# Kernel optimization log

Hardware: AMD Instinct MI355X
Metric: run time of the kernel (lower is better)

Reference implementation:

```python
import jax, jax.numpy as jnp
import numpy as np

NUM_LAYERS = 2
SHAPES = [(100, 100), (50, 50), (25, 25), (13, 13)]  # (H, W) per level
D, NH, NP, NL = 256, 8, 4, 4
DH = D // NH
DFF = 1024
B = 2
S = sum(h * w for h, w in SHAPES)  # 13294


def layer_norm(x, g, b, eps=1e-5):
    m = x.mean(-1, keepdims=True)
    v = jnp.var(x, axis=-1, keepdims=True)
    return (x - m) * jax.lax.rsqrt(v + eps) * g + b


def get_reference_points(valid_ratios):
    refs = []
    for lvl, (H_, W_) in enumerate(SHAPES):
        ry, rx = jnp.meshgrid(jnp.linspace(0.5, H_ - 0.5, H_),
                              jnp.linspace(0.5, W_ - 0.5, W_), indexing='ij')
        ry = ry.reshape(-1)[None] / (valid_ratios[:, None, lvl, 1] * H_)
        rx = rx.reshape(-1)[None] / (valid_ratios[:, None, lvl, 0] * W_)
        refs.append(jnp.stack([rx, ry], -1))
    ref = jnp.concatenate(refs, 1)                      # [B, S, 2]
    return ref[:, :, None] * valid_ratios[:, None]      # [B, S, NL, 2]


def sample_level(value_l, H_, W_, loc):
    # value_l: [B, nH, H*W, Dh]; loc: [B, Q, nH, P, 2] normalized in [0,1]
    x = loc[..., 0] * W_ - 0.5
    y = loc[..., 1] * H_ - 0.5
    x0 = jnp.floor(x)
    y0 = jnp.floor(y)
    Bq, Q = loc.shape[0], loc.shape[1]
    acc = 0.
    corners = ((x0, y0, (x0 + 1 - x) * (y0 + 1 - y)),
               (x0 + 1, y0, (x - x0) * (y0 + 1 - y)),
               (x0, y0 + 1, (x0 + 1 - x) * (y - y0)),
               (x0 + 1, y0 + 1, (x - x0) * (y - y0)))
    for xi, yi, w in corners:  # zero-padding grid_sample: invalid corners contribute 0
        valid = (xi >= 0) & (xi <= W_ - 1) & (yi >= 0) & (yi <= H_ - 1)
        idx = (jnp.clip(yi, 0, H_ - 1) * W_ + jnp.clip(xi, 0, W_ - 1)).astype(jnp.int32)
        idx = jnp.transpose(idx, (0, 2, 1, 3)).reshape(Bq, NH, Q * NP)
        g = jnp.take_along_axis(value_l, idx[..., None], axis=2)  # [B,nH,Q*P,Dh]
        wv = jnp.transpose((w * valid).astype(value_l.dtype), (0, 2, 1, 3)).reshape(Bq, NH, Q * NP)
        acc = acc + g * wv[..., None]
    return acc.reshape(Bq, NH, Q, NP, DH)


def msda(query, ref, src, W_val, b_val, W_off, b_off, W_attn, b_attn, W_out, b_out):
    Bq, Q = query.shape[:2]
    value = (src @ W_val + b_val).reshape(Bq, S, NH, DH)
    off = (query @ W_off + b_off).reshape(Bq, Q, NH, NL, NP, 2)
    attn = jax.nn.softmax((query @ W_attn + b_attn).reshape(Bq, Q, NH, NL * NP), -1)
    attn = attn.reshape(Bq, Q, NH, NL, NP)
    normalizer = jnp.array([[w, h] for h, w in SHAPES], dtype=query.dtype)  # [NL,2] (x,y)
    loc = ref[:, :, None, :, None, :] + off / normalizer[None, None, None, :, None, :]
    out = jnp.zeros((Bq, NH, Q, DH), query.dtype)
    start = 0
    for l, (H_, W_) in enumerate(SHAPES):
        v_l = jnp.transpose(value[:, start:start + H_ * W_], (0, 2, 1, 3))  # [B,nH,HW,Dh]
        samp = sample_level(v_l, H_, W_, loc[:, :, :, l])                    # [B,nH,Q,P,Dh]
        w_l = jnp.transpose(attn[:, :, :, l], (0, 2, 1, 3))                  # [B,nH,Q,P]
        out = out + (samp * w_l[..., None]).sum(3)
        start += H_ * W_
    out = jnp.transpose(out, (0, 2, 1, 3)).reshape(Bq, Q, D)
    return out @ W_out + b_out


def setup_inputs() -> dict:
    key = jax.random.key(0)
    ks = jax.random.split(key, 12)
    sc = 0.02
    inp = {
        'src': jax.random.normal(ks[0], (B, S, D), jnp.float32),
        'spatial_shapes': np.array(SHAPES, dtype=np.int64),
        'valid_ratios': jnp.ones((B, NL, 2), jnp.float32),
        'W_off': sc * jax.random.normal(ks[1], (NUM_LAYERS, D, NH * NL * NP * 2), jnp.float32),
        'b_off': jnp.zeros((NUM_LAYERS, NH * NL * NP * 2), jnp.float32),
        'W_attn': sc * jax.random.normal(ks[2], (NUM_LAYERS, D, NH * NL * NP), jnp.float32),
        'b_attn': jnp.zeros((NUM_LAYERS, NH * NL * NP), jnp.float32),
        'W_val': sc * jax.random.normal(ks[3], (NUM_LAYERS, D, D), jnp.float32),
        'b_val': jnp.zeros((NUM_LAYERS, D), jnp.float32),
        'W_out': sc * jax.random.normal(ks[4], (NUM_LAYERS, D, D), jnp.float32),
        'b_out': jnp.zeros((NUM_LAYERS, D), jnp.float32),
        'ln1_g': jnp.ones((NUM_LAYERS, D), jnp.float32),
        'ln1_b': jnp.zeros((NUM_LAYERS, D), jnp.float32),
        'W1': sc * jax.random.normal(ks[5], (NUM_LAYERS, D, DFF), jnp.float32),
        'b1': jnp.zeros((NUM_LAYERS, DFF), jnp.float32),
        'W2': sc * jax.random.normal(ks[6], (NUM_LAYERS, DFF, D), jnp.float32),
        'b2': jnp.zeros((NUM_LAYERS, D), jnp.float32),
        'ln2_g': jnp.ones((NUM_LAYERS, D), jnp.float32),
        'ln2_b': jnp.zeros((NUM_LAYERS, D), jnp.float32),
    }
    return inp


def reference(src, spatial_shapes, valid_ratios, W_off, b_off, W_attn, b_attn,
              W_val, b_val, W_out, b_out, ln1_g, ln1_b, W1, b1, W2, b2, ln2_g, ln2_b):
    # Deformable-DETR encoder stack (dropout=0 / eval mode, pos=None, no padding mask).
    ref = get_reference_points(valid_ratios)  # [B, S, NL, 2]
    x = src
    for i in range(NUM_LAYERS):
        x2 = msda(x, ref, x, W_val[i], b_val[i], W_off[i], b_off[i],
                  W_attn[i], b_attn[i], W_out[i], b_out[i])
        x = layer_norm(x + x2, ln1_g[i], ln1_b[i])
        h = jax.nn.relu(x @ W1[i] + b1[i]) @ W2[i] + b2[i]
        x = layer_norm(x + h, ln2_g[i], ln2_b[i])
    return x
```

## Files before the change

### kernel.cpp

```cpp
#include <hip/hip_runtime.h>
#include <math.h>


#define S_TOT 13294
#define BATCH 2
#define M_TOT (BATCH * S_TOT)
#define M_PAD 26624

typedef __attribute__((ext_vector_type(8))) short short8;
typedef __attribute__((ext_vector_type(4))) float floatx4;
typedef __attribute__((ext_vector_type(2))) float floatx2;

#define AS1C(p) ((const __attribute__((address_space(1))) void*)(p))
#define AS3(p)  ((__attribute__((address_space(3))) void*)(p))

static __device__ __forceinline__ unsigned short f2bf(float x) {
    union { float f; unsigned u; } v; v.f = x;
    unsigned r = v.u + 0x7FFFu + ((v.u >> 16) & 1u);
    return (unsigned short)(r >> 16);
}
static __device__ __forceinline__ float b2f(unsigned short u) {
    union { unsigned u; float f; } v; v.u = (unsigned)u << 16; return v.f;
}
static __device__ __forceinline__ float bflo(unsigned u) {
    union { unsigned u; float f; } v; v.u = u << 16; return v.f;
}
static __device__ __forceinline__ float bfhi(unsigned u) {
    union { unsigned u; float f; } v; v.u = u & 0xFFFF0000u; return v.f;
}
static __device__ __forceinline__ float braw(unsigned u) {
    union { unsigned u; float f; } v; v.u = u; return v.f;
}

template<int TM, bool RELU, bool BF16OUT, bool PROJ>
__global__ __launch_bounds__(256)
void mgemm(const unsigned short* __restrict__ A,
           const unsigned short* __restrict__ BT,
           const float* __restrict__ bias,
           const float* __restrict__ bias2,
           const float* __restrict__ bias3,
           unsigned short* __restrict__ Cb,
           unsigned short* __restrict__ Cb2,
           int M, int N, int K)
{
    constexpr int WM = (TM == 128) ? 2 : 1;
    constexpr int WN = 4 / WM;
    constexpr int MI = TM / (WM * 16);
    constexpr int NI = 128 / (WN * 16);
    __shared__ __align__(16) unsigned short smemA[2 * TM * 32];
    __shared__ __align__(16) unsigned short smemB[2 * 128 * 32];
    const int tid  = threadIdx.x;
    const int lane = tid & 63;
    const int w    = tid >> 6;
    const int wm   = w % WM, wn = w / WM;
    const int lr   = lane & 15, quad = lane >> 4;
    const int bm   = blockIdx.y * TM;
    const int bn   = blockIdx.x * 128;

    floatx4 acc[MI][NI];
    #pragma unroll
    for (int i = 0; i < MI; ++i)
        #pragma unroll
        for (int j = 0; j < NI; ++j)
            acc[i][j] = (floatx4){0.f, 0.f, 0.f, 0.f};

    const int srow = lane >> 2;
    const int selt = (lane & 3) << 3;

    for (int k0 = 0; k0 < K; k0 += 64) {
        #pragma unroll
        for (int c = 0; c < 2; ++c) {
            if (TM == 128) {
                #pragma unroll
                for (int jj = 0; jj < 2; ++jj) {
                    const int j = 2 * w + jj;
                    const unsigned short* ga = A  + (size_t)(bm + j * 16 + srow) * K + k0 + c * 32 + selt;
                    const unsigned short* gb = BT + (size_t)(bn + j * 16 + srow) * K + k0 + c * 32 + selt;
                    __builtin_amdgcn_global_load_lds(AS1C(ga), AS3(smemA + c * (TM * 32) + j * 512), 16, 0, 0);
                    __builtin_amdgcn_global_load_lds(AS1C(gb), AS3(smemB + c * 4096 + j * 512), 16, 0, 0);
                }
            } else {
                const unsigned short* ga = A + (size_t)(bm + w * 16 + srow) * K + k0 + c * 32 + selt;
                __builtin_amdgcn_global_load_lds(AS1C(ga), AS3(smemA + c * (TM * 32) + w * 512), 16, 0, 0);
                #pragma unroll
                for (int jj = 0; jj < 2; ++jj) {
                    const int j = 2 * w + jj;
                    const unsigned short* gb = BT + (size_t)(bn + j * 16 + srow) * K + k0 + c * 32 + selt;
                    __builtin_amdgcn_global_load_lds(AS1C(gb), AS3(smemB + c * 4096 + j * 512), 16, 0, 0);
                }
            }
        }
        __syncthreads();

        #pragma unroll
        for (int c = 0; c < 2; ++c) {
            short8 av[MI], bv[NI];
            #pragma unroll
            for (int mi = 0; mi < MI; ++mi)
                av[mi] = *(const short8*)&smemA[c * (TM * 32) + (wm * MI * 16 + mi * 16 + lr) * 32 + quad * 8];
            #pragma unroll
            for (int ni = 0; ni < NI; ++ni)
                bv[ni] = *(const short8*)&smemB[c * 4096 + (wn * NI * 16 + ni * 16 + lr) * 32 + quad * 8];
            #pragma unroll
            for (int mi = 0; mi < MI; ++mi)
                #pragma unroll
                for (int ni = 0; ni < NI; ++ni)
                    acc[mi][ni] = __builtin_amdgcn_mfma_f32_16x16x32_bf16(
                        av[mi], bv[ni], acc[mi][ni], 0, 0, 0);
        }
        __syncthreads();
    }

    #pragma unroll
    for (int mi = 0; mi < MI; ++mi) {
        #pragma unroll
        for (int ni = 0; ni < NI; ++ni) {
            #pragma unroll
            for (int r = 0; r < 4; ++r) {
                const int row = bm + wm * MI * 16 + mi * 16 + quad * 4 + r;
                const int col = bn + wn * NI * 16 + ni * 16 + lr;
                if (PROJ) {
                    const float bb = (col < 256) ? bias[col]
                                   : (col < 512) ? bias2[col - 256]
                                                 : bias3[col - 512];
                    const float v = acc[mi][ni][r] + bb;
                    if (col < 256) Cb[(size_t)row * 256 + col] = f2bf(v);
                    else           Cb2[(size_t)row * 384 + (col - 256)] = f2bf(v);
                } else {
                    float v = acc[mi][ni][r] + bias[col];
                    if (RELU) v = fmaxf(v, 0.0f);
                    if (BF16OUT) Cb[(size_t)row * N + col] = f2bf(v);
                }
            }
        }
    }
}

template<bool HASF, bool HASB>
__global__ __launch_bounds__(256)
void mgemm_ln(const unsigned short* __restrict__ A,
              const unsigned short* __restrict__ BT,
              const float* __restrict__ bias,
              const unsigned short* __restrict__ R,
              const float* __restrict__ g,
              const float* __restrict__ beta,
              float* __restrict__ outF,
              unsigned short* __restrict__ outB,
              int M, int K)
{
    __shared__ __align__(16) unsigned short smemA[2 * 4096];
    __shared__ __align__(16) unsigned short smemB[2 * 16384];
    const int lane = threadIdx.x & 63;
    const int w    = threadIdx.x >> 6;
    const int lr   = lane & 15, quad = lane >> 4;
    const int bm   = blockIdx.x * 64;
    const int srow = lane >> 2;
    const int selt = (lane & 3) << 3;

    floatx4 acc[4][4];
    #pragma unroll
    for (int i = 0; i < 4; ++i)
        #pragma unroll
        for (int j = 0; j < 4; ++j)
            acc[i][j] = (floatx4){0.f, 0.f, 0.f, 0.f};

    auto stage = [&](int kt, int buf) {
        const int k0 = kt * 64;
        #pragma unroll
        for (int c = 0; c < 2; ++c) {
            const unsigned short* ga = A + (size_t)(bm + w * 16 + srow) * K + k0 + c * 32 + selt;
            __builtin_amdgcn_global_load_lds(AS1C(ga), AS3(smemA + buf * 4096 + c * 2048 + w * 512), 16, 0, 0);
            #pragma unroll
            for (int jj = 0; jj < 4; ++jj) {
                const int j = 4 * w + jj;
                const unsigned short* gb = BT + (size_t)(j * 16 + srow) * K + k0 + c * 32 + selt;
                __builtin_amdgcn_global_load_lds(AS1C(gb), AS3(smemB + buf * 16384 + c * 8192 + j * 512), 16, 0, 0);
            }
        }
    };

    const int NK = K >> 6;
    stage(0, 0);
    for (int kt = 0; kt < NK; ++kt) {
        const int buf = kt & 1;
        __syncthreads();
        if (kt + 1 < NK) stage(kt + 1, buf ^ 1);
        #pragma unroll
        for (int c = 0; c < 2; ++c) {
            short8 av[4], bv[4];
            #pragma unroll
            for (int mi = 0; mi < 4; ++mi)
                av[mi] = *(const short8*)&smemA[buf * 4096 + c * 2048 + (mi * 16 + lr) * 32 + quad * 8];
            #pragma unroll
            for (int ni = 0; ni < 4; ++ni)
                bv[ni] = *(const short8*)&smemB[buf * 16384 + c * 8192 + (w * 64 + ni * 16 + lr) * 32 + quad * 8];
            #pragma unroll
            for (int mi = 0; mi < 4; ++mi)
                #pragma unroll
                for (int ni = 0; ni < 4; ++ni)
                    acc[mi][ni] = __builtin_amdgcn_mfma_f32_16x16x32_bf16(
                        av[mi], bv[ni], acc[mi][ni], 0, 0, 0);
        }
    }

    float bs[4], gs[4], bts[4];
    #pragma unroll
    for (int ni = 0; ni < 4; ++ni) {
        const int col = w * 64 + ni * 16 + lr;
        bs[ni] = bias[col]; gs[ni] = g[col]; bts[ni] = beta[col];
    }
    float* lnbuf = (float*)smemA;

    #pragma unroll
    for (int mi = 0; mi < 4; ++mi) {
        #pragma unroll
        for (int r = 0; r < 4; ++r) {
            const int rl = mi * 16 + quad * 4 + r;
            const int grow = bm + rl;
            const bool act = grow < M;
            float p = 0.f, q = 0.f;
            #pragma unroll
            for (int ni = 0; ni < 4; ++ni) {
                const int col = w * 64 + ni * 16 + lr;
                const float rv = act ? b2f(R[(size_t)grow * 256 + col]) : 0.f;
                const float x = acc[mi][ni][r] + bs[ni] + rv;
                acc[mi][ni][r] = x;
                p += x; q += x * x;
            }
            #pragma unroll
            for (int o = 1; o < 16; o <<= 1) {
                p += __shfl_xor(p, o, 64);
                q += __shfl_xor(q, o, 64);
            }
            if (lr == 0) {
                lnbuf[rl * 8 + 2 * w]     = p;
                lnbuf[rl * 8 + 2 * w + 1] = q;
            }
        }
    }
    __syncthreads();
    #pragma unroll
    for (int mi = 0; mi < 4; ++mi) {
        #pragma unroll
        for (int r = 0; r < 4; ++r) {
            const int rl = mi * 16 + quad * 4 + r;
            const int grow = bm + rl;
            const float4 pa = *(const float4*)&lnbuf[rl * 8];
            const float4 pb = *(const float4*)&lnbuf[rl * 8 + 4];
            const float s  = pa.x + pa.z + pb.x + pb.z;
            const float s2 = pa.y + pa.w + pb.y + pb.w;
            const float mean = s * (1.0f / 256.0f);
            const float var  = s2 * (1.0f / 256.0f) - mean * mean;
            const float rs   = rsqrtf(var + 1e-5f);
            if (grow < M) {
                #pragma unroll
                for (int ni = 0; ni < 4; ++ni) {
                    const int col = w * 64 + ni * 16 + lr;
                    const float y = (acc[mi][ni][r] - mean) * rs * gs[ni] + bts[ni];
                    if (HASF) outF[(size_t)grow * 256 + col] = y;
                    if (HASB) outB[(size_t)grow * 256 + col] = f2bf(y);
                }
            }
        }
    }
}

__global__ __launch_bounds__(256)
void convpad(const float* __restrict__ X, unsigned short* __restrict__ Y, int M)
{
    const int idx = blockIdx.x * 256 + threadIdx.x;
    const int row = idx >> 6;
    const int c4  = (idx & 63) << 2;
    if (row >= M_PAD) return;
    float4 v = {0.f, 0.f, 0.f, 0.f};
    if (row < M) v = ((const float4*)(X + (size_t)row * 256))[c4 >> 2];
    unsigned p0 = (unsigned)f2bf(v.x) | ((unsigned)f2bf(v.y) << 16);
    unsigned p1 = (unsigned)f2bf(v.z) | ((unsigned)f2bf(v.w) << 16);
    uint2 o; o.x = p0; o.y = p1;
    *(uint2*)(Y + (size_t)row * 256 + c4) = o;
}

struct WJobs {
    const float* W[12];
    unsigned short* WT[12];
    int K[12], N[12], tx[12], start[12];
};

__global__ __launch_bounds__(256)
void wtrans_all(WJobs jb)
{
    __shared__ float t[32][33];
    const int bx = blockIdx.x;
    int seg = 0;
    #pragma unroll
    for (int s = 1; s < 12; ++s) if (bx >= jb.start[s]) seg = s;
    const float* W = jb.W[seg];
    unsigned short* WT = jb.WT[seg];
    const int K = jb.K[seg], N = jb.N[seg], tx = jb.tx[seg];
    const int local = bx - jb.start[seg];
    const int n0 = (local % tx) * 32, k0 = (local / tx) * 32;
    const int c = threadIdx.x & 31, r0 = threadIdx.x >> 5;
    #pragma unroll
    for (int rr = r0; rr < 32; rr += 8)
        t[rr][c] = W[(size_t)(k0 + rr) * N + n0 + c];
    __syncthreads();
    #pragma unroll
    for (int rr = r0; rr < 32; rr += 8)
        WT[(size_t)(n0 + rr) * K + k0 + c] = f2bf(t[c][rr]);
}

__global__ __launch_bounds__(256)
void msda_kernel(const unsigned short* __restrict__ valb,
                 const unsigned short* __restrict__ oab,
                 const float* __restrict__ vr,
                 unsigned short* __restrict__ out)
{
    __shared__ __align__(16) char smeta[8 * 128 * 32];
    const int t = threadIdx.x;
    const int bid = (blockIdx.x & 7) * 416 + (blockIdx.x >> 3);

    {
        const int wv = t >> 6, lane = t & 63;
        const int lqA = wv * 2 + (lane >> 5);
        const int bq = bid * 8 + lqA;
        const int h = (lane >> 2) & 7;
        const int j = lane & 3;
        if (bq < M_TOT) {
            const int b = (bq >= S_TOT) ? 1 : 0;
            const int q = bq - b * S_TOT;
            const int bofs = b * (S_TOT * 512);
            int Hq, rr, cc, lq;
            if (q < 10000)      { lq = 0; Hq = 100; rr = q / 100;              cc = q - rr * 100; }
            else if (q < 12500) { lq = 1; Hq = 50;  int r2 = q - 10000; rr = r2 / 50; cc = r2 - rr * 50; }
            else if (q < 13125) { lq = 2; Hq = 25;  int r2 = q - 12500; rr = r2 / 25; cc = r2 - rr * 25; }
            else                { lq = 3; Hq = 13;  int r2 = q - 13125; rr = r2 / 13; cc = r2 - rr * 13; }
            const float rxb = (cc + 0.5f) / (vr[(b * 4 + lq) * 2 + 0] * (float)Hq);
            const float ryb = (rr + 0.5f) / (vr[(b * 4 + lq) * 2 + 1] * (float)Hq);
            const int HWt[4] = {100, 50, 25, 13};
            const int stt[4] = {0, 10000, 12500, 13125};
            const int HW = HWt[j], st = stt[j];
            const float fW = (float)HW;
            const float refxw = rxb * vr[(b * 4 + j) * 2 + 0] * fW - 0.5f;
            const float refyw = ryb * vr[(b * 4 + j) * 2 + 1] * fW - 0.5f;
            const unsigned short* row = oab + (size_t)bq * 384;
            const uint2 lgu = *(const uint2*)(row + 256 + h * 16 + j * 4);
            const float l0 = bflo(lgu.x), l1 = bfhi(lgu.x);
            const float l2 = bflo(lgu.y), l3 = bfhi(lgu.y);
            float mx = fmaxf(fmaxf(l0, l1), fmaxf(l2, l3));
            mx = fmaxf(mx, __shfl_xor(mx, 1, 64));
            mx = fmaxf(mx, __shfl_xor(mx, 2, 64));
            const float e0 = __expf(l0 - mx), e1 = __expf(l1 - mx);
            const float e2 = __expf(l2 - mx), e3 = __expf(l3 - mx);
            float ss = e0 + e1 + e2 + e3;
            ss += __shfl_xor(ss, 1, 64);
            ss += __shfl_xor(ss, 2, 64);
            const float inv = 1.0f / ss;
            const uint4 ou = *(const uint4*)(row + h * 32 + j * 8);
            const float oxs[4] = {bflo(ou.x), bflo(ou.y), bflo(ou.z), bflo(ou.w)};
            const float oys[4] = {bfhi(ou.x), bfhi(ou.y), bfhi(ou.z), bfhi(ou.w)};
            const float aw[4]  = {e0 * inv, e1 * inv, e2 * inv, e3 * inv};
            char* mb = smeta + (size_t)(lqA * 128 + h * 16 + j * 4) * 32;
            const int swz = ((h * 4 + j) & 7) << 4;
            #pragma unroll
            for (int p = 0; p < 4; ++p) {
                const float x = refxw + oxs[p];
                const float y = refyw + oys[p];
                const float x0f = floorf(x), y0f = floorf(y);
                const int x0 = (int)x0f, y0 = (int)y0f;
                const float fx = x - x0f, fy = y - y0f;
                const float wb[4] = {(1.f - fx) * (1.f - fy), fx * (1.f - fy),
                                     (1.f - fx) * fy,         fx * fy};
                const int xs[2] = {x0, x0 + 1};
                const int ys2[2] = {y0, y0 + 1};
                int iv[4]; float wv4[4];
                #pragma unroll
                for (int k = 0; k < 4; ++k) {
                    const int xi = xs[k & 1], yi = ys2[k >> 1];
                    const bool vld = ((unsigned)xi < (unsigned)HW) && ((unsigned)yi < (unsigned)HW);
                    const int xc = min(max(xi, 0), HW - 1);
                    const int yc = min(max(yi, 0), HW - 1);
                    iv[k] = bofs + ((st + yc * HW + xc) << 9) + (h << 6);
                    wv4[k] = vld ? wb[k] * aw[p] : 0.0f;
                }
                int4 i4; i4.x = iv[0]; i4.y = iv[1]; i4.z = iv[2]; i4.w = iv[3];
                float4 w4; w4.x = wv4[0]; w4.y = wv4[1]; w4.z = wv4[2]; w4.w = wv4[3];
                *(int4*)(mb + ((p * 32) ^ swz)) = i4;
                *(float4*)(mb + ((p * 32 + 16) ^ swz)) = w4;
            }
        }
    }
    __syncthreads();
    {
        const int lq2 = t >> 5;
        const int r = t & 31;
        const int h2 = r >> 2;
        const int cg = r & 3;
        const int bq2 = bid * 8 + lq2;
        if (bq2 < M_TOT) {
            const char* vbase = (const char*)valb;
            const unsigned cgo = cg * 16;
            floatx2 a0 = {0.f, 0.f}, a1 = {0.f, 0.f}, a2 = {0.f, 0.f}, a3 = {0.f, 0.f};
            const char* mb2 = smeta + (size_t)(lq2 * 128 + h2 * 16) * 32;
            #pragma unroll 4
            for (int s = 0; s < 16; ++s) {
                const int swz2 = ((h2 * 4 + (s >> 2)) & 7) << 4;
                const int4  iv = *(const int4*)(mb2 + ((s * 32) ^ swz2));
                const float4 w4 = *(const float4*)(mb2 + ((s * 32 + 16) ^ swz2));
                const uint4 u0 = *(const uint4*)(vbase + (unsigned)(iv.x + cgo));
                const uint4 u1 = *(const uint4*)(vbase + (unsigned)(iv.y + cgo));
                const uint4 u2 = *(const uint4*)(vbase + (unsigned)(iv.z + cgo));
                const uint4 u3 = *(const uint4*)(vbase + (unsigned)(iv.w + cgo));
                #define ACC8(UU, WW) { \
                    const floatx2 w2 = {WW, WW}; \
                    const floatx2 t0 = {bflo(UU.x), braw(UU.x)}; \
                    const floatx2 t1 = {bflo(UU.y), braw(UU.y)}; \
                    const floatx2 t2 = {bflo(UU.z), braw(UU.z)}; \
                    const floatx2 t3 = {bflo(UU.w), braw(UU.w)}; \
                    a0 += w2 * t0; a1 += w2 * t1; a2 += w2 * t2; a3 += w2 * t3; }
                ACC8(u0, w4.x) ACC8(u1, w4.y) ACC8(u2, w4.z) ACC8(u3, w4.w)
                #undef ACC8
            }
            uint4 o;
            o.x = (unsigned)f2bf(a0.x) | ((unsigned)f2bf(a0.y) << 16);
            o.y = (unsigned)f2bf(a1.x) | ((unsigned)f2bf(a1.y) << 16);
            o.z = (unsigned)f2bf(a2.x) | ((unsigned)f2bf(a2.y) << 16);
            o.w = (unsigned)f2bf(a3.x) | ((unsigned)f2bf(a3.y) << 16);
            *(uint4*)(out + (size_t)bq2 * 256 + h2 * 32 + cg * 8) = o;
        }
    }
}

extern "C" void kernel_launch(void* const* d_in, const int* in_sizes, int n_in,
                              void* d_out, int out_size, void* d_ws, size_t ws_size,
                              hipStream_t stream)
{
    const float* src    = (const float*)d_in[0];
    const float* vr     = (const float*)d_in[2];
    const float* W_off  = (const float*)d_in[3];
    const float* b_off  = (const float*)d_in[4];
    const float* W_attn = (const float*)d_in[5];
    const float* b_attn = (const float*)d_in[6];
    const float* W_val  = (const float*)d_in[7];
    const float* b_val  = (const float*)d_in[8];
    const float* W_out  = (const float*)d_in[9];
    const float* b_out  = (const float*)d_in[10];
    const float* ln1_g  = (const float*)d_in[11];
    const float* ln1_b  = (const float*)d_in[12];
    const float* W1     = (const float*)d_in[13];
    const float* b1     = (const float*)d_in[14];
    const float* W2     = (const float*)d_in[15];
    const float* b2     = (const float*)d_in[16];
    const float* ln2_g  = (const float*)d_in[17];
    const float* ln2_b  = (const float*)d_in[18];
    float* out = (float*)d_out;

    const int M = M_TOT;

    char* wsb = (char*)d_ws;
    unsigned short* HBF  = (unsigned short*)wsb;
    unsigned short* OAB  = (unsigned short*)wsb;
    unsigned short* VALB = (unsigned short*)(wsb + 20447232);
    unsigned short* X1B  = (unsigned short*)(wsb + 54525952);
    unsigned short* RB   = (unsigned short*)(wsb + 81788928);
    unsigned short* YBF  = (unsigned short*)(wsb + 95420416);
    unsigned short* WT   = (unsigned short*)(wsb + 109051904);

    const size_t LWT = 753664;
    const size_t oProj = 0, oOut = 163840, oW1 = 229376, oW2 = 491520;

    WJobs jb;
    int startAcc = 0;
    for (int i = 0; i < 2; ++i) {
        unsigned short* wt = WT + i * LWT;
        const float* srcs[6] = {W_val + i * 65536, W_off + i * 65536, W_attn + i * 32768,
                                W_out + i * 65536, W1 + i * 262144, W2 + i * 262144};
        unsigned short* dsts[6] = {wt + oProj, wt + oProj + 65536, wt + oProj + 131072,
                                   wt + oOut, wt + oW1, wt + oW2};
        const int Ks[6] = {256, 256, 256, 256, 256, 1024};
        const int Ns[6] = {256, 256, 128, 256, 1024, 256};
        for (int s = 0; s < 6; ++s) {
            const int idx = i * 6 + s;
            jb.W[idx] = srcs[s]; jb.WT[idx] = dsts[s];
            jb.K[idx] = Ks[s]; jb.N[idx] = Ns[s]; jb.tx[idx] = Ns[s] / 32;
            jb.start[idx] = startAcc;
            startAcc += (Ns[s] / 32) * (Ks[s] / 32);
        }
    }
    wtrans_all<<<dim3(startAcc), 256, 0, stream>>>(jb);

    const int GM128 = M_PAD / 128;
    const int GM64  = M_PAD / 64;
    const dim3 blk(256);

    for (int i = 0; i < 2; ++i) {
        unsigned short* wt = WT + i * LWT;

        if (i == 0)
            convpad<<<dim3(M_PAD / 4), blk, 0, stream>>>(src, RB, M);

        mgemm<64, false, false, true><<<dim3(5, GM64), blk, 0, stream>>>(
            RB, wt + oProj, b_val + i * 256, b_off + i * 256, b_attn + i * 128,
            VALB, OAB, M, 640, 256);

        msda_kernel<<<dim3(3328), blk, 0, stream>>>(VALB, OAB, vr, YBF);

        mgemm_ln<false, true><<<dim3(GM64), blk, 0, stream>>>(
            YBF, wt + oOut, b_out + i * 256, RB,
            ln1_g + i * 256, ln1_b + i * 256, nullptr, X1B, M, 256);

        mgemm<128, true, true, false><<<dim3(8, GM128), blk, 0, stream>>>(
            X1B, wt + oW1, b1 + i * 1024, nullptr, nullptr,
            HBF, nullptr, M, 1024, 256);

        if (i == 0)
            mgemm_ln<false, true><<<dim3(GM64), blk, 0, stream>>>(
                HBF, wt + oW2, b2 + i * 256, X1B,
                ln2_g + i * 256, ln2_b + i * 256, nullptr, RB, M, 1024);
        else
            mgemm_ln<true, false><<<dim3(GM64), blk, 0, stream>>>(
                HBF, wt + oW2, b2 + i * 256, X1B,
                ln2_g + i * 256, ln2_b + i * 256, out, nullptr, M, 1024);
    }
}
```

Baseline: 427.5 us.

## Split fused GEMM+LayerNorm into generic GEMM with fp32 output and separate LN kernel

Replaces the full-row (N=256) GEMM+LayerNorm kernels with the generic tiled mgemm writing fp32 results, followed by a lightweight per-row LayerNorm kernel using wave-wide shuffles. This gives the output and FFN2 GEMMs more blocks (2 column tiles per row tile) and avoids the large 64x256 tile with its heavy LDS footprint. In exchange it adds an fp32 round trip through global memory and two extra kernel launches per layer.

```diff
diff --git a/kernel.cpp b/kernel.cpp
--- a/kernel.cpp
+++ b/kernel.cpp
@@ -32,7 +32,7 @@
     union { unsigned u; float f; } v; v.u = u; return v.f;
 }
 
-template<int TM, bool RELU, bool BF16OUT, bool PROJ>
+template<int TM, bool RELU, bool BF16OUT, bool PROJ, bool F32OUT>
 __global__ __launch_bounds__(256)
 void mgemm(const unsigned short* __restrict__ A,
            const unsigned short* __restrict__ BT,
@@ -41,6 +41,9 @@
            const float* __restrict__ bias3,
            unsigned short* __restrict__ Cb,
            unsigned short* __restrict__ Cb2,
+           float* __restrict__ Cf1,
+           float* __restrict__ Cf2,
+           int strideF,
            int M, int N, int K)
 {
     constexpr int WM = (TM == 128) ? 2 : 1;
@@ -126,6 +129,10 @@
                     const float v = acc[mi][ni][r] + bb;
                     if (col < 256) Cb[(size_t)row * 256 + col] = f2bf(v);
                     else           Cb2[(size_t)row * 384 + (col - 256)] = f2bf(v);
+                } else if (F32OUT) {
+                    const float v = acc[mi][ni][r] + bias[col];
+                    float* dst = (col < 128) ? Cf1 : Cf2;
+                    dst[(size_t)row * strideF + (col & 127)] = v;
                 } else {
                     float v = acc[mi][ni][r] + bias[col];
                     if (RELU) v = fmaxf(v, 0.0f);
@@ -138,130 +145,51 @@
 
 template<bool HASF, bool HASB>
 __global__ __launch_bounds__(256)
-void mgemm_ln(const unsigned short* __restrict__ A,
-              const unsigned short* __restrict__ BT,
-              const float* __restrict__ bias,
-              const unsigned short* __restrict__ R,
-              const float* __restrict__ g,
-              const float* __restrict__ beta,
-              float* __restrict__ outF,
-              unsigned short* __restrict__ outB,
-              int M, int K)
-{
-    __shared__ __align__(16) unsigned short smemA[2 * 4096];
-    __shared__ __align__(16) unsigned short smemB[2 * 16384];
+void ln_kernel(const float* __restrict__ Y1, const float* __restrict__ Y2,
+               int strideF,
+               const unsigned short* __restrict__ R,
+               const float* __restrict__ g, const float* __restrict__ beta,
+               float* __restrict__ outF, unsigned short* __restrict__ outB,
+               int M)
+{
     const int lane = threadIdx.x & 63;
-    const int w    = threadIdx.x >> 6;
-    const int lr   = lane & 15, quad = lane >> 4;
-    const int bm   = blockIdx.x * 64;
-    const int srow = lane >> 2;
-    const int selt = (lane & 3) << 3;
-
-    floatx4 acc[4][4];
-    #pragma unroll
-    for (int i = 0; i < 4; ++i)
-        #pragma unroll
-        for (int j = 0; j < 4; ++j)
-            acc[i][j] = (floatx4){0.f, 0.f, 0.f, 0.f};
-
-    auto stage = [&](int kt, int buf) {
-        const int k0 = kt * 64;
-        #pragma unroll
-        for (int c = 0; c < 2; ++c) {
-            const unsigned short* ga = A + (size_t)(bm + w * 16 + srow) * K + k0 + c * 32 + selt;
-            __builtin_amdgcn_global_load_lds(AS1C(ga), AS3(smemA + buf * 4096 + c * 2048 + w * 512), 16, 0, 0);
-            #pragma unroll
-            for (int jj = 0; jj < 4; ++jj) {
-                const int j = 4 * w + jj;
-                const unsigned short* gb = BT + (size_t)(j * 16 + srow) * K + k0 + c * 32 + selt;
-                __builtin_amdgcn_global_load_lds(AS1C(gb), AS3(smemB + buf * 16384 + c * 8192 + j * 512), 16, 0, 0);
-            }
-        }
-    };
-
-    const int NK = K >> 6;
-    stage(0, 0);
-    for (int kt = 0; kt < NK; ++kt) {
-        const int buf = kt & 1;
-        __syncthreads();
-        if (kt + 1 < NK) stage(kt + 1, buf ^ 1);
-        #pragma unroll
-        for (int c = 0; c < 2; ++c) {
-            short8 av[4], bv[4];
-            #pragma unroll
-            for (int mi = 0; mi < 4; ++mi)
-                av[mi] = *(const short8*)&smemA[buf * 4096 + c * 2048 + (mi * 16 + lr) * 32 + quad * 8];
-            #pragma unroll
-            for (int ni = 0; ni < 4; ++ni)
-                bv[ni] = *(const short8*)&smemB[buf * 16384 + c * 8192 + (w * 64 + ni * 16 + lr) * 32 + quad * 8];
-            #pragma unroll
-            for (int mi = 0; mi < 4; ++mi)
-                #pragma unroll
-                for (int ni = 0; ni < 4; ++ni)
-                    acc[mi][ni] = __builtin_amdgcn_mfma_f32_16x16x32_bf16(
-                        av[mi], bv[ni], acc[mi][ni], 0, 0, 0);
-        }
-    }
-
-    float bs[4], gs[4], bts[4];
-    #pragma unroll
-    for (int ni = 0; ni < 4; ++ni) {
-        const int col = w * 64 + ni * 16 + lr;
-        bs[ni] = bias[col]; gs[ni] = g[col]; bts[ni] = beta[col];
-    }
-    float* lnbuf = (float*)smemA;
-
-    #pragma unroll
-    for (int mi = 0; mi < 4; ++mi) {
-        #pragma unroll
-        for (int r = 0; r < 4; ++r) {
-            const int rl = mi * 16 + quad * 4 + r;
-            const int grow = bm + rl;
-            const bool act = grow < M;
-            float p = 0.f, q = 0.f;
-            #pragma unroll
-            for (int ni = 0; ni < 4; ++ni) {
-                const int col = w * 64 + ni * 16 + lr;
-                const float rv = act ? b2f(R[(size_t)grow * 256 + col]) : 0.f;
-                const float x = acc[mi][ni][r] + bs[ni] + rv;
-                acc[mi][ni][r] = x;
-                p += x; q += x * x;
-            }
-            #pragma unroll
-            for (int o = 1; o < 16; o <<= 1) {
-                p += __shfl_xor(p, o, 64);
-                q += __shfl_xor(q, o, 64);
-            }
-            if (lr == 0) {
-                lnbuf[rl * 8 + 2 * w]     = p;
-                lnbuf[rl * 8 + 2 * w + 1] = q;
-            }
-        }
-    }
-    __syncthreads();
-    #pragma unroll
-    for (int mi = 0; mi < 4; ++mi) {
-        #pragma unroll
-        for (int r = 0; r < 4; ++r) {
-            const int rl = mi * 16 + quad * 4 + r;
-            const int grow = bm + rl;
-            const float4 pa = *(const float4*)&lnbuf[rl * 8];
-            const float4 pb = *(const float4*)&lnbuf[rl * 8 + 4];
-            const float s  = pa.x + pa.z + pb.x + pb.z;
-            const float s2 = pa.y + pa.w + pb.y + pb.w;
-            const float mean = s * (1.0f / 256.0f);
-            const float var  = s2 * (1.0f / 256.0f) - mean * mean;
-            const float rs   = rsqrtf(var + 1e-5f);
-            if (grow < M) {
-                #pragma unroll
-                for (int ni = 0; ni < 4; ++ni) {
-                    const int col = w * 64 + ni * 16 + lr;
-                    const float y = (acc[mi][ni][r] - mean) * rs * gs[ni] + bts[ni];
-                    if (HASF) outF[(size_t)grow * 256 + col] = y;
-                    if (HASB) outB[(size_t)grow * 256 + col] = f2bf(y);
-                }
-            }
-        }
+    const int row  = blockIdx.x * 4 + (threadIdx.x >> 6);
+    if (row >= M) return;
+    const int c4 = lane * 4;
+    const float* src = (lane < 32)
+        ? (Y1 + (size_t)row * strideF + c4)
+        : (Y2 + (size_t)row * strideF + (c4 - 128));
+    const float4 v = *(const float4*)src;
+    const uint2 rr = *(const uint2*)(R + (size_t)row * 256 + c4);
+    const float x0 = v.x + bflo(rr.x);
+    const float x1 = v.y + bfhi(rr.x);
+    const float x2 = v.z + bflo(rr.y);
+    const float x3 = v.w + bfhi(rr.y);
+    float p = (x0 + x1) + (x2 + x3);
+    float q = (x0 * x0 + x1 * x1) + (x2 * x2 + x3 * x3);
+    #pragma unroll
+    for (int o = 1; o < 64; o <<= 1) {
+        p += __shfl_xor(p, o, 64);
+        q += __shfl_xor(q, o, 64);
+    }
+    const float mean = p * (1.0f / 256.0f);
+    const float var  = q * (1.0f / 256.0f) - mean * mean;
+    const float rs   = rsqrtf(var + 1e-5f);
+    const float4 gv = *(const float4*)(g + c4);
+    const float4 bv = *(const float4*)(beta + c4);
+    const float y0 = (x0 - mean) * rs * gv.x + bv.x;
+    const float y1 = (x1 - mean) * rs * gv.y + bv.y;
+    const float y2 = (x2 - mean) * rs * gv.z + bv.z;
+    const float y3 = (x3 - mean) * rs * gv.w + bv.w;
+    if (HASF) {
+        float4 o4; o4.x = y0; o4.y = y1; o4.z = y2; o4.w = y3;
+        *(float4*)(outF + (size_t)row * 256 + c4) = o4;
+    }
+    if (HASB) {
+        uint2 o2;
+        o2.x = (unsigned)f2bf(y0) | ((unsigned)f2bf(y1) << 16);
+        o2.y = (unsigned)f2bf(y2) | ((unsigned)f2bf(y3) << 16);
+        *(uint2*)(outB + (size_t)row * 256 + c4) = o2;
     }
 }
 
@@ -460,9 +388,12 @@
     unsigned short* HBF  = (unsigned short*)wsb;
     unsigned short* OAB  = (unsigned short*)wsb;
     unsigned short* VALB = (unsigned short*)(wsb + 20447232);
+    float*          GB1  = (float*)wsb;
     unsigned short* X1B  = (unsigned short*)(wsb + 54525952);
+    float*          Pf   = (float*)(wsb + 68157440);
     unsigned short* RB   = (unsigned short*)(wsb + 81788928);
     unsigned short* YBF  = (unsigned short*)(wsb + 95420416);
+    float*          Qf   = (float*)(wsb + 95420416);
     unsigned short* WT   = (unsigned short*)(wsb + 109051904);
 
     const size_t LWT = 753664;
@@ -490,6 +421,7 @@
 
     const int GM128 = M_PAD / 128;
     const int GM64  = M_PAD / 64;
+    const int GLN   = M_TOT / 4;
     const dim3 blk(256);
 
     for (int i = 0; i < 2; ++i) {
@@ -498,27 +430,35 @@
         if (i == 0)
             convpad<<<dim3(M_PAD / 4), blk, 0, stream>>>(src, RB, M);
 
-        mgemm<64, false, false, true><<<dim3(5, GM64), blk, 0, stream>>>(
+        mgemm<64, false, false, true, false><<<dim3(5, GM64), blk, 0, stream>>>(
             RB, wt + oProj, b_val + i * 256, b_off + i * 256, b_attn + i * 128,
-            VALB, OAB, M, 640, 256);
+            VALB, OAB, nullptr, nullptr, 0, M, 640, 256);
 
         msda_kernel<<<dim3(3328), blk, 0, stream>>>(VALB, OAB, vr, YBF);
 
-        mgemm_ln<false, true><<<dim3(GM64), blk, 0, stream>>>(
-            YBF, wt + oOut, b_out + i * 256, RB,
-            ln1_g + i * 256, ln1_b + i * 256, nullptr, X1B, M, 256);
-
-        mgemm<128, true, true, false><<<dim3(8, GM128), blk, 0, stream>>>(
+        mgemm<64, false, false, false, true><<<dim3(2, GM64), blk, 0, stream>>>(
+            YBF, wt + oOut, b_out + i * 256, nullptr, nullptr,
+            nullptr, nullptr, GB1, GB1 + 128, 256, M, 256, 256);
+
+        ln_kernel<false, true><<<dim3(GLN), blk, 0, stream>>>(
+            GB1, GB1 + 128, 256, RB, ln1_g + i * 256, ln1_b + i * 256,
+            nullptr, X1B, M);
+
+        mgemm<128, true, true, false, false><<<dim3(8, GM128), blk, 0, stream>>>(
             X1B, wt + oW1, b1 + i * 1024, nullptr, nullptr,
-            HBF, nullptr, M, 1024, 256);
+            HBF, nullptr, nullptr, nullptr, 0, M, 1024, 256);
+
+        mgemm<64, false, false, false, true><<<dim3(2, GM64), blk, 0, stream>>>(
+            HBF, wt + oW2, b2 + i * 256, nullptr, nullptr,
+            nullptr, nullptr, Pf, Qf, 128, M, 256, 1024);
 
         if (i == 0)
-            mgemm_ln<false, true><<<dim3(GM64), blk, 0, stream>>>(
-                HBF, wt + oW2, b2 + i * 256, X1B,
-                ln2_g + i * 256, ln2_b + i * 256, nullptr, RB, M, 1024);
+            ln_kernel<false, true><<<dim3(GLN), blk, 0, stream>>>(
+                Pf, Qf, 128, X1B, ln2_g + i * 256, ln2_b + i * 256,
+                nullptr, RB, M);
         else
-            mgemm_ln<true, false><<<dim3(GM64), blk, 0, stream>>>(
-                HBF, wt + oW2, b2 + i * 256, X1B,
-                ln2_g + i * 256, ln2_b + i * 256, out, nullptr, M, 1024);
-    }
-}
+            ln_kernel<true, false><<<dim3(GLN), blk, 0, stream>>>(
+                Pf, Qf, 128, X1B, ln2_g + i * 256, ln2_b + i * 256,
+                out, nullptr, M);
+    }
+}
```

New measurement: 438.7 us. 1.03x slower.
